# Performance work log

Measured on AMD Instinct MI355X. Metric: run time of the kernel, lower is better.

The kernel has to match this reference:

```python
import jax, jax.numpy as jnp
import numpy as np

B, LN, LT, D, DIN, H = 8, 64, 256, 1024, 2048, 4
LN_EPS = 1e-5
F16_EPS = float(np.finfo(np.float16).eps)


def setup_inputs() -> dict:
    key = jax.random.key(0)
    ks = jax.random.split(key, 16)
    n = lambda k, sh: jax.random.normal(k, sh, dtype=jnp.float32)
    s = 0.02
    z = lambda sh: jnp.zeros(sh, jnp.float32)
    return {
        "text_embeds": n(ks[0], (B, LT, D)),
        "node_embeds": n(ks[1], (B, LN, D)),
        "Wq": n(ks[2], (D, H * D)) * s, "bq": z((H * D,)),
        "Wk": n(ks[3], (D, H * D)) * s, "bk": z((H * D,)),
        "Wv": n(ks[4], (D, H * D)) * s, "bv": z((H * D,)),
        "Wo": n(ks[5], (H * D, D)) * s, "bo": z((D,)),
        "ln_g": jnp.ones((D,), jnp.float32), "ln_b": z((D,)),
        "aqW": n(ks[6], (D, D)) * s, "aqb": z((D,)),
        "akW": n(ks[7], (D, D)) * s, "akb": z((D,)),
        "att_v": n(ks[8], (D,)) * (1.0 / np.sqrt(D)),
        "att_b": z((D,)),
        "dp1W": n(ks[9], (D, DIN // 2)) * s, "dp1b": z((DIN // 2,)),
        "dp2W": n(ks[10], (DIN // 2, DIN)) * s, "dp2b": z((DIN,)),
        "gnn_mask": jax.random.randint(ks[11], (B, LN), 0, 2),
        "lm_mask": jax.random.randint(ks[12], (B, LT), 0, 2),
    }


def _forward(text_embeds, node_embeds, Wq, bq, Wk, bk, Wv, bv, Wo, bo, ln_g, ln_b,
             aqW, aqb, akW, akb, att_v, att_b, dp1W, dp1b, dp2W, dp2b,
             gnn_mask, lm_mask):
    x = node_embeds  # (B, LN, D)

    # ---- selfAttention_prompt: each of 4 heads has full width D ----
    def heads(w, b):
        return (x @ w + b).reshape(B, LN, H, D).transpose(0, 2, 1, 3)  # (B,H,LN,D)

    Q, K, V = heads(Wq, bq), heads(Wk, bk), heads(Wv, bv)
    A = jnp.einsum('bhqd,bhkd->bhqk', Q, K) / jnp.sqrt(jnp.float32(D))
    A = jnp.where(gnn_mask[:, None, None, :] == 0, -jnp.inf, A)
    alpha = jax.nn.softmax(A, axis=-1)
    out = jnp.einsum('bhqk,bhkd->bhqd', alpha, V)
    out = out.transpose(0, 2, 1, 3).reshape(B, LN, H * D)
    out = out @ Wo + bo + x
    # LayerNorm (torch default eps=1e-5)
    mu = out.mean(-1, keepdims=True)
    var = ((out - mu) ** 2).mean(-1, keepdims=True)
    H2 = (out - mu) / jnp.sqrt(var + LN_EPS) * ln_g + ln_b  # (B, LN, D)

    # ---- AdditiveAttention (Bahdanau): value_proj is unused in the original ----
    q = H2 @ aqW + aqb            # (B, LN, D)
    k = text_embeds @ akW + akb   # (B, LT, D)
    e = jnp.einsum('bqkd,d->bqk',
                   jnp.tanh(q[:, :, None, :] + k[:, None, :, :] + att_b), att_v)
    e = jnp.where(lm_mask[:, None, :] == 0, -jnp.inf, e)
    w = jax.nn.softmax(e, axis=-1)            # (B, LN, LT)
    H3 = jnp.einsum('bqk,bkd->bqd', w, text_embeds)  # context with raw V

    # ---- filter_Pool: masked mean over nodes ----
    m = gnn_mask.astype(H3.dtype)[:, :, None]
    cnt = jnp.clip(m.sum(1), F16_EPS, None)   # (B, 1)
    H4 = (H3 * m).sum(1) / cnt                # (B, D)

    # ---- domain projector (exact GELU like torch) ----
    Z = jax.nn.gelu(H4 @ dp1W + dp1b, approximate=False) @ dp2W + dp2b
    return Z  # (B, DIN)


def reference(text_embeds, node_embeds, Wq, bq, Wk, bk, Wv, bv, Wo, bo, ln_g, ln_b,
              aqW, aqb, akW, akb, att_v, att_b, dp1W, dp1b, dp2W, dp2b,
              gnn_mask, lm_mask):
    return _forward(text_embeds, node_embeds, Wq, bq, Wk, bk, Wv, bv, Wo, bo,
                    ln_g, ln_b, aqW, aqb, akW, akb, att_v, att_b,
                    dp1W, dp1b, dp2W, dp2b, gnn_mask, lm_mask)
```

## Files before the change

### kernel.cpp

```cpp
#include <hip/hip_runtime.h>
#include <hip/hip_bf16.h>
#include <math.h>

#define NB 8
#define LNN 64
#define LTN 256
#define DD 1024
#define NH 4
#define HDD 4096
#define DINN 2048
#define DHN 1024

#define C_TANH 2.8853900817779268f

typedef __bf16 bf16x8 __attribute__((ext_vector_type(8)));
typedef float f32x4 __attribute__((ext_vector_type(4)));

__device__ __forceinline__ ushort f2b(float f) {
  unsigned int u = __builtin_bit_cast(unsigned int, f);
  u = (u + 0x7FFFu + ((u >> 16) & 1u)) >> 16;
  return (ushort)u;
}

__global__ __launch_bounds__(256) void prep(const float* __restrict__ node,
                                            ushort* __restrict__ node_bf,
                                            const float* __restrict__ text,
                                            ushort* __restrict__ text_bf,
                                            const float* __restrict__ Wq,
                                            const float* __restrict__ Wk,
                                            const float* __restrict__ Wv,
                                            const float* __restrict__ Wo,
                                            const float* __restrict__ aqW,
                                            const float* __restrict__ akW,
                                            ushort* __restrict__ TwtQKV,
                                            ushort* __restrict__ TwtWo,
                                            ushort* __restrict__ TwtAQ) {
  int bid = blockIdx.x;
  int t = threadIdx.x;
  if (bid < 1280) {
    const float* in;
    ushort* out;
    int i;
    if (bid < 256) { in = node; out = node_bf; i = (bid * 256 + t) * 8; }
    else { in = text; out = text_bf; i = ((bid - 256) * 256 + t) * 8; }
    float4 a = *(const float4*)(in + i);
    float4 b = *(const float4*)(in + i + 4);
    ushort4 o0 = {f2b(a.x), f2b(a.y), f2b(a.z), f2b(a.w)};
    ushort4 o1 = {f2b(b.x), f2b(b.y), f2b(b.z), f2b(b.w)};
    *(ushort4*)(out + i) = o0;
    *(ushort4*)(out + i + 4) = o1;
    return;
  }
  bid -= 1280;
  const float* W;
  ushort* dst0;
  int K, N, tt;
  if (bid < 3072) {
    int z = bid >> 10;
    tt = bid & 1023;
    W = (z == 0) ? Wq : ((z == 1) ? Wk : Wv);
    dst0 = TwtQKV + (size_t)z * DD * HDD;
    K = DD; N = HDD;
  } else if (bid < 4096) {
    tt = bid - 3072; W = Wo; dst0 = TwtWo; K = HDD; N = DD;
  } else if (bid < 4352) {
    tt = bid - 4096; W = aqW; dst0 = TwtAQ; K = DD; N = DD;
  } else {
    tt = bid - 4352; W = akW; dst0 = TwtAQ + (size_t)DD * DD; K = DD; N = DD;
  }
  int ntn = N >> 6;
  int n0 = (tt % ntn) << 6, k0 = (tt / ntn) << 6;
  __shared__ float tf[64][65];
  int r = t >> 2, c4 = (t & 3) * 16;
  const float* src = W + (size_t)(k0 + r) * N + n0 + c4;
  float4 v0 = *(const float4*)(src);
  float4 v1 = *(const float4*)(src + 4);
  float4 v2 = *(const float4*)(src + 8);
  float4 v3 = *(const float4*)(src + 12);
  *(float4*)&tf[r][c4] = v0;
  *(float4*)&tf[r][c4 + 4] = v1;
  *(float4*)&tf[r][c4 + 8] = v2;
  *(float4*)&tf[r][c4 + 12] = v3;
  __syncthreads();
  int nl = t >> 2, kc = (t & 3) * 16;
  ushort tmp[16];
#pragma unroll
  for (int j = 0; j < 16; ++j) tmp[j] = f2b(tf[kc + j][nl]);
  ushort* dst = dst0 + (size_t)(n0 + nl) * K + k0 + kc;
  *(uint4*)(dst) = *(uint4*)&tmp[0];
  *(uint4*)(dst + 8) = *(uint4*)&tmp[8];
}

__global__ __launch_bounds__(256) void gemm_qkv3(const ushort* __restrict__ A,
                                                 const ushort* __restrict__ BtB,
                                                 const float* __restrict__ b0,
                                                 const float* __restrict__ b1,
                                                 const float* __restrict__ b2,
                                                 ushort* __restrict__ o0,
                                                 ushort* __restrict__ o1,
                                                 ushort* __restrict__ o2,
                                                 int M, int N, int K) {
  int z = blockIdx.z;
  const ushort* Bt = BtB + (size_t)z * N * K;
  const float* bias = (z == 0) ? b0 : ((z == 1) ? b1 : b2);
  ushort* Cout = (z == 0) ? o0 : ((z == 1) ? o1 : o2);
  __shared__ ushort Als[64 * 64];
  __shared__ ushort Bls[128 * 64];
  int tid = threadIdx.x;
  int m0 = blockIdx.y << 6, n0 = blockIdx.x << 7;
  int srow = tid >> 3, su = tid & 7;
  int sx = (su ^ (srow & 7)) * 8;
  const ushort* ga = A + (size_t)(m0 + srow) * K + su * 8;
  const ushort* gb = Bt + (size_t)(n0 + srow) * K + su * 8;
  int wa0 = srow * 64 + sx, wa1 = (srow + 32) * 64 + sx;
  int wb2 = (srow + 64) * 64 + sx, wb3 = (srow + 96) * 64 + sx;
  const size_t rs32 = (size_t)32 * K;
  int lane = tid & 63, w = tid >> 6;
  int wm = w >> 1, wn = w & 1;
  int r = lane & 15, kg = lane >> 4;
  f32x4 acc[2][4] = {};
  uint4 pa0 = *(const uint4*)(ga);
  uint4 pa1 = *(const uint4*)(ga + rs32);
  uint4 pb0 = *(const uint4*)(gb);
  uint4 pb1 = *(const uint4*)(gb + rs32);
  uint4 pb2 = *(const uint4*)(gb + 2 * rs32);
  uint4 pb3 = *(const uint4*)(gb + 3 * rs32);
  for (int k0 = 0; k0 < K; k0 += 64) {
    __syncthreads();
    *(uint4*)&Als[wa0] = pa0; *(uint4*)&Als[wa1] = pa1;
    *(uint4*)&Bls[wa0] = pb0; *(uint4*)&Bls[wa1] = pb1;
    *(uint4*)&Bls[wb2] = pb2; *(uint4*)&Bls[wb3] = pb3;
    __syncthreads();
    int kn = k0 + 64;
    if (kn < K) {
      pa0 = *(const uint4*)(ga + kn);
      pa1 = *(const uint4*)(ga + rs32 + kn);
      pb0 = *(const uint4*)(gb + kn);
      pb1 = *(const uint4*)(gb + rs32 + kn);
      pb2 = *(const uint4*)(gb + 2 * rs32 + kn);
      pb3 = *(const uint4*)(gb + 3 * rs32 + kn);
    }
#pragma unroll
    for (int h = 0; h < 2; ++h) {
      int sa = ((h * 4 + kg) ^ (r & 7)) * 8;
      bf16x8 af[2], bfr[4];
#pragma unroll
      for (int m = 0; m < 2; ++m)
        af[m] = *(const bf16x8*)&Als[(wm * 32 + m * 16 + r) * 64 + sa];
#pragma unroll
      for (int n = 0; n < 4; ++n)
        bfr[n] = *(const bf16x8*)&Bls[(wn * 64 + n * 16 + r) * 64 + sa];
#pragma unroll
      for (int m = 0; m < 2; ++m)
#pragma unroll
        for (int n = 0; n < 4; ++n)
          acc[m][n] = __builtin_amdgcn_mfma_f32_16x16x32_bf16(af[m], bfr[n], acc[m][n], 0, 0, 0);
    }
  }
#pragma unroll
  for (int m = 0; m < 2; ++m)
#pragma unroll
    for (int n = 0; n < 4; ++n) {
      f32x4 a = acc[m][n];
#pragma unroll
      for (int v = 0; v < 4; ++v) {
        int row = m0 + wm * 32 + m * 16 + kg * 4 + v;
        int col = n0 + wn * 64 + n * 16 + r;
        Cout[(size_t)row * N + col] = f2b(a[v] + bias[col]);
      }
    }
}

__global__ __launch_bounds__(256) void gemm_wo_split(const ushort* __restrict__ A,
                                                     const ushort* __restrict__ Bt,
                                                     float* __restrict__ P,
                                                     int M, int N, int K) {
  __shared__ ushort Als[64 * 64];
  __shared__ ushort Bls[128 * 64];
  int tid = threadIdx.x;
  int m0 = blockIdx.y << 6, n0 = blockIdx.x << 7;
  int Ks = K >> 2, kbase = blockIdx.z * Ks;
  int srow = tid >> 3, su = tid & 7;
  int sx = (su ^ (srow & 7)) * 8;
  const ushort* ga = A + (size_t)(m0 + srow) * K + kbase + su * 8;
  const ushort* gb = Bt + (size_t)(n0 + srow) * K + kbase + su * 8;
  int wa0 = srow * 64 + sx, wa1 = (srow + 32) * 64 + sx;
  int wb2 = (srow + 64) * 64 + sx, wb3 = (srow + 96) * 64 + sx;
  const size_t rs32 = (size_t)32 * K;
  int lane = tid & 63, w = tid >> 6;
  int wm = w >> 1, wn = w & 1;
  int r = lane & 15, kg = lane >> 4;
  f32x4 acc[2][4] = {};
  uint4 pa0 = *(const uint4*)(ga);
  uint4 pa1 = *(const uint4*)(ga + rs32);
  uint4 pb0 = *(const uint4*)(gb);
  uint4 pb1 = *(const uint4*)(gb + rs32);
  uint4 pb2 = *(const uint4*)(gb + 2 * rs32);
  uint4 pb3 = *(const uint4*)(gb + 3 * rs32);
  for (int k0 = 0; k0 < Ks; k0 += 64) {
    __syncthreads();
    *(uint4*)&Als[wa0] = pa0; *(uint4*)&Als[wa1] = pa1;
    *(uint4*)&Bls[wa0] = pb0; *(uint4*)&Bls[wa1] = pb1;
    *(uint4*)&Bls[wb2] = pb2; *(uint4*)&Bls[wb3] = pb3;
    __syncthreads();
    int kn = k0 + 64;
    if (kn < Ks) {
      pa0 = *(const uint4*)(ga + kn);
      pa1 = *(const uint4*)(ga + rs32 + kn);
      pb0 = *(const uint4*)(gb + kn);
      pb1 = *(const uint4*)(gb + rs32 + kn);
      pb2 = *(const uint4*)(gb + 2 * rs32 + kn);
      pb3 = *(const uint4*)(gb + 3 * rs32 + kn);
    }
#pragma unroll
    for (int h = 0; h < 2; ++h) {
      int sa = ((h * 4 + kg) ^ (r & 7)) * 8;
      bf16x8 af[2], bfr[4];
#pragma unroll
      for (int m = 0; m < 2; ++m)
        af[m] = *(const bf16x8*)&Als[(wm * 32 + m * 16 + r) * 64 + sa];
#pragma unroll
      for (int n = 0; n < 4; ++n)
        bfr[n] = *(const bf16x8*)&Bls[(wn * 64 + n * 16 + r) * 64 + sa];
#pragma unroll
      for (int m = 0; m < 2; ++m)
#pragma unroll
        for (int n = 0; n < 4; ++n)
          acc[m][n] = __builtin_amdgcn_mfma_f32_16x16x32_bf16(af[m], bfr[n], acc[m][n], 0, 0, 0);
    }
  }
#pragma unroll
  for (int m = 0; m < 2; ++m)
#pragma unroll
    for (int n = 0; n < 4; ++n) {
      f32x4 a = acc[m][n];
#pragma unroll
      for (int v = 0; v < 4; ++v) {
        int row = m0 + wm * 32 + m * 16 + kg * 4 + v;
        int col = n0 + wn * 64 + n * 16 + r;
        P[((size_t)blockIdx.z * M + row) * N + col] = a[v];
      }
    }
}

__global__ __launch_bounds__(256) void gemm_aqak(const ushort* __restrict__ H2,
                                                 const ushort* __restrict__ Tbf,
                                                 const ushort* __restrict__ TwtAQ,
                                                 const float* __restrict__ aqb,
                                                 const float* __restrict__ akb,
                                                 const float* __restrict__ attb,
                                                 float* __restrict__ QBu,
                                                 float* __restrict__ KAB,
                                                 int N, int K) {
  __shared__ ushort Als[64 * 64];
  __shared__ ushort Bls[128 * 64];
  int tid = threadIdx.x;
  int gm0 = blockIdx.y << 6, n0 = blockIdx.x << 7;
  const ushort* Abase;
  const ushort* Bt;
  const float* bias;
  const float* bias2;
  float* Obase;
  if (gm0 < 512) {
    Abase = H2 + (size_t)gm0 * K;
    Bt = TwtAQ;
    bias = aqb; bias2 = nullptr;
    Obase = QBu + (size_t)gm0 * N;
  } else {
    Abase = Tbf + (size_t)(gm0 - 512) * K;
    Bt = TwtAQ + (size_t)N * K;
    bias = akb; bias2 = attb;
    Obase = KAB + (size_t)(gm0 - 512) * N;
  }
  int srow = tid >> 3, su = tid & 7;
  int sx = (su ^ (srow & 7)) * 8;
  const ushort* ga = Abase + (size_t)srow * K + su * 8;
  const ushort* gb = Bt + (size_t)(n0 + srow) * K + su * 8;
  int wa0 = srow * 64 + sx, wa1 = (srow + 32) * 64 + sx;
  int wb2 = (srow + 64) * 64 + sx, wb3 = (srow + 96) * 64 + sx;
  const size_t rs32 = (size_t)32 * K;
  int lane = tid & 63, w = tid >> 6;
  int wm = w >> 1, wn = w & 1;
  int r = lane & 15, kg = lane >> 4;
  f32x4 acc[2][4] = {};
  uint4 pa0 = *(const uint4*)(ga);
  uint4 pa1 = *(const uint4*)(ga + rs32);
  uint4 pb0 = *(const uint4*)(gb);
  uint4 pb1 = *(const uint4*)(gb + rs32);
  uint4 pb2 = *(const uint4*)(gb + 2 * rs32);
  uint4 pb3 = *(const uint4*)(gb + 3 * rs32);
  for (int k0 = 0; k0 < K; k0 += 64) {
    __syncthreads();
    *(uint4*)&Als[wa0] = pa0; *(uint4*)&Als[wa1] = pa1;
    *(uint4*)&Bls[wa0] = pb0; *(uint4*)&Bls[wa1] = pb1;
    *(uint4*)&Bls[wb2] = pb2; *(uint4*)&Bls[wb3] = pb3;
    __syncthreads();
    int kn = k0 + 64;
    if (kn < K) {
      pa0 = *(const uint4*)(ga + kn);
      pa1 = *(const uint4*)(ga + rs32 + kn);
      pb0 = *(const uint4*)(gb + kn);
      pb1 = *(const uint4*)(gb + rs32 + kn);
      pb2 = *(const uint4*)(gb + 2 * rs32 + kn);
      pb3 = *(const uint4*)(gb + 3 * rs32 + kn);
    }
#pragma unroll
    for (int h = 0; h < 2; ++h) {
      int sa = ((h * 4 + kg) ^ (r & 7)) * 8;
      bf16x8 af[2], bfr[4];
#pragma unroll
      for (int m = 0; m < 2; ++m)
        af[m] = *(const bf16x8*)&Als[(wm * 32 + m * 16 + r) * 64 + sa];
#pragma unroll
      for (int n = 0; n < 4; ++n)
        bfr[n] = *(const bf16x8*)&Bls[(wn * 64 + n * 16 + r) * 64 + sa];
#pragma unroll
      for (int m = 0; m < 2; ++m)
#pragma unroll
        for (int n = 0; n < 4; ++n)
          acc[m][n] = __builtin_amdgcn_mfma_f32_16x16x32_bf16(af[m], bfr[n], acc[m][n], 0, 0, 0);
    }
  }
#pragma unroll
  for (int m = 0; m < 2; ++m)
#pragma unroll
    for (int n = 0; n < 4; ++n) {
      f32x4 a = acc[m][n];
#pragma unroll
      for (int v = 0; v < 4; ++v) {
        int lrow = wm * 32 + m * 16 + kg * 4 + v;
        int col = n0 + wn * 64 + n * 16 + r;
        float x = a[v] + bias[col];
        if (bias2) x += bias2[col];
        Obase[(size_t)lrow * N + col] = x * C_TANH;
      }
    }
}

__global__ __launch_bounds__(256) void wo_ln(const float* __restrict__ P,
                                             const float* __restrict__ bo,
                                             const float* __restrict__ node,
                                             const float* __restrict__ g,
                                             const float* __restrict__ be,
                                             ushort* __restrict__ Y) {
  int row = blockIdx.x, tid = threadIdx.x;
  int c = tid * 4;
  const size_t MN = (size_t)512 * 1024;
  size_t o = (size_t)row * DD + c;
  float4 v0 = *(const float4*)(P + o);
  float4 v1 = *(const float4*)(P + MN + o);
  float4 v2 = *(const float4*)(P + 2 * MN + o);
  float4 v3 = *(const float4*)(P + 3 * MN + o);
  float4 rv = *(const float4*)(node + o);
  float4 bv = *(const float4*)(bo + c);
  float4 v;
  v.x = v0.x + v1.x + v2.x + v3.x + rv.x + bv.x;
  v.y = v0.y + v1.y + v2.y + v3.y + rv.y + bv.y;
  v.z = v0.z + v1.z + v2.z + v3.z + rv.z + bv.z;
  v.w = v0.w + v1.w + v2.w + v3.w + rv.w + bv.w;
  float s = v.x + v.y + v.z + v.w;
  float ss = v.x * v.x + v.y * v.y + v.z * v.z + v.w * v.w;
  for (int o2 = 32; o2; o2 >>= 1) {
    s += __shfl_xor(s, o2, 64);
    ss += __shfl_xor(ss, o2, 64);
  }
  __shared__ float rb_[8];
  int lane = tid & 63, w = tid >> 6;
  if (lane == 0) { rb_[w] = s; rb_[4 + w] = ss; }
  __syncthreads();
  s = rb_[0] + rb_[1] + rb_[2] + rb_[3];
  ss = rb_[4] + rb_[5] + rb_[6] + rb_[7];
  float mu = s * (1.f / 1024.f);
  float var = ss * (1.f / 1024.f) - mu * mu;
  float rstd = rsqrtf(var + 1e-5f);
  ushort4 o4;
  o4.x = f2b((v.x - mu) * rstd * g[c + 0] + be[c + 0]);
  o4.y = f2b((v.y - mu) * rstd * g[c + 1] + be[c + 1]);
  o4.z = f2b((v.z - mu) * rstd * g[c + 2] + be[c + 2]);
  o4.w = f2b((v.w - mu) * rstd * g[c + 3] + be[c + 3]);
  *(ushort4*)(Y + (size_t)row * DD + c) = o4;
}

__global__ __launch_bounds__(256) void attn_qk(const ushort* __restrict__ Qb,
                                               const ushort* __restrict__ Kb,
                                               float* __restrict__ Sp) {
  int bh = blockIdx.x, ks = blockIdx.y;
  int b = bh >> 2;
  size_t base = ((size_t)b * LNN) * HDD + (size_t)(bh & 3) * DD + ks * 128;
  __shared__ ushort Als[64 * 64];
  __shared__ ushort Bls[64 * 64];
  int tid = threadIdx.x;
  int srow = tid >> 2, su0 = (tid & 3) * 2;
  const ushort* ga = Qb + base + (size_t)srow * HDD + su0 * 8;
  const ushort* gb = Kb + base + (size_t)srow * HDD + su0 * 8;
  int wa0 = srow * 64 + ((su0) ^ (srow & 7)) * 8;
  int wa1 = srow * 64 + ((su0 + 1) ^ (srow & 7)) * 8;
  int lane = tid & 63, w = tid >> 6;
  int wm = w >> 1, wn = w & 1;
  int r = lane & 15, kg = lane >> 4;
  f32x4 acc[2][2] = {};
  uint4 pa0 = *(const uint4*)(ga);
  uint4 pa1 = *(const uint4*)(ga + 8);
  uint4 pb0 = *(const uint4*)(gb);
  uint4 pb1 = *(const uint4*)(gb + 8);
  for (int k0 = 0; k0 < 128; k0 += 64) {
    __syncthreads();
    *(uint4*)&Als[wa0] = pa0; *(uint4*)&Als[wa1] = pa1;
    *(uint4*)&Bls[wa0] = pb0; *(uint4*)&Bls[wa1] = pb1;
    __syncthreads();
    if (k0 == 0) {
      pa0 = *(const uint4*)(ga + 64);
      pa1 = *(const uint4*)(ga + 64 + 8);
      pb0 = *(const uint4*)(gb + 64);
      pb1 = *(const uint4*)(gb + 64 + 8);
    }
#pragma unroll
    for (int h = 0; h < 2; ++h) {
      int sa = ((h * 4 + kg) ^ (r & 7)) * 8;
      bf16x8 af[2], bfr[2];
#pragma unroll
      for (int m = 0; m < 2; ++m)
        af[m] = *(const bf16x8*)&Als[(wm * 32 + m * 16 + r) * 64 + sa];
#pragma unroll
      for (int n = 0; n < 2; ++n)
        bfr[n] = *(const bf16x8*)&Bls[(wn * 32 + n * 16 + r) * 64 + sa];
#pragma unroll
      for (int m = 0; m < 2; ++m)
#pragma unroll
        for (int n = 0; n < 2; ++n)
          acc[m][n] = __builtin_amdgcn_mfma_f32_16x16x32_bf16(af[m], bfr[n], acc[m][n], 0, 0, 0);
    }
  }
  float* out = Sp + ((size_t)ks * 32 + bh) * 4096;
#pragma unroll
  for (int m = 0; m < 2; ++m)
#pragma unroll
    for (int n = 0; n < 2; ++n) {
      f32x4 a = acc[m][n];
#pragma unroll
      for (int v = 0; v < 4; ++v) {
        int row = wm * 32 + m * 16 + kg * 4 + v;
        int col = wn * 32 + n * 16 + r;
        out[row * 64 + col] = a[v];
      }
    }
}

__global__ __launch_bounds__(256) void attn_pv(const float* __restrict__ Sp,
                                               const ushort* __restrict__ Vb,
                                               const int* __restrict__ gmask,
                                               ushort* __restrict__ AO) {
  int bid = blockIdx.x;
  int bh = bid >> 3, dt = bid & 7;
  int b = bh >> 2;
  int d0 = dt * 128;
  size_t base = ((size_t)b * LNN) * HDD + (size_t)(bh & 3) * DD;
  __shared__ float S[64][68];
  __shared__ ushort Pls[64 * 72];
  __shared__ ushort Vt[128 * 72];
  int tid = threadIdx.x;
  int lane = tid & 63, w = tid >> 6;
  {
    int fbase = tid * 16;
    float a[16];
#pragma unroll
    for (int i = 0; i < 16; i += 4) {
      float4 v = *(const float4*)(Sp + (size_t)bh * 4096 + fbase + i);
      a[i] = v.x; a[i + 1] = v.y; a[i + 2] = v.z; a[i + 3] = v.w;
    }
#pragma unroll
    for (int ks = 1; ks < 8; ++ks) {
      const float* p = Sp + ((size_t)ks * 32 + bh) * 4096 + fbase;
#pragma unroll
      for (int i = 0; i < 16; i += 4) {
        float4 v = *(const float4*)(p + i);
        a[i] += v.x; a[i + 1] += v.y; a[i + 2] += v.z; a[i + 3] += v.w;
      }
    }
    int q = fbase >> 6, k = fbase & 63;
#pragma unroll
    for (int i = 0; i < 16; ++i) S[q][k + i] = a[i];
  }
  {
    int kq = lane, dq = w * 32;
    const ushort* src = Vb + base + (size_t)kq * HDD + d0 + dq;
    uint4 v0 = *(const uint4*)src;
    uint4 v1 = *(const uint4*)(src + 8);
    uint4 v2 = *(const uint4*)(src + 16);
    uint4 v3 = *(const uint4*)(src + 24);
    ushort tmp[32];
    *(uint4*)&tmp[0] = v0; *(uint4*)&tmp[8] = v1;
    *(uint4*)&tmp[16] = v2; *(uint4*)&tmp[24] = v3;
#pragma unroll
    for (int j = 0; j < 32; ++j) Vt[(dq + j) * 72 + kq] = tmp[j];
  }
  __syncthreads();
  bool valid = gmask[b * LNN + lane] != 0;
  for (int i = 0; i < 16; ++i) {
    int q = w * 16 + i;
    float v = valid ? S[q][lane] * 0.03125f : -__builtin_inff();
    float mx = v;
    for (int o = 32; o; o >>= 1) mx = fmaxf(mx, __shfl_xor(mx, o, 64));
    float e = valid ? __expf(v - mx) : 0.f;
    float s = e;
    for (int o = 32; o; o >>= 1) s += __shfl_xor(s, o, 64);
    Pls[q * 72 + lane] = f2b(__fdividef(e, s));
  }
  __syncthreads();
  int wm = w >> 1, wn = w & 1;
  int r = lane & 15, kg = lane >> 4;
  f32x4 acc[2][4] = {};
#pragma unroll
  for (int h = 0; h < 2; ++h) {
    int ko = h * 32 + kg * 8;
    bf16x8 af[2], bfr[4];
#pragma unroll
    for (int m = 0; m < 2; ++m)
      af[m] = *(const bf16x8*)&Pls[(wm * 32 + m * 16 + r) * 72 + ko];
#pragma unroll
    for (int n = 0; n < 4; ++n)
      bfr[n] = *(const bf16x8*)&Vt[(wn * 64 + n * 16 + r) * 72 + ko];
#pragma unroll
    for (int m = 0; m < 2; ++m)
#pragma unroll
      for (int n = 0; n < 4; ++n)
        acc[m][n] = __builtin_amdgcn_mfma_f32_16x16x32_bf16(af[m], bfr[n], acc[m][n], 0, 0, 0);
  }
#pragma unroll
  for (int m = 0; m < 2; ++m)
#pragma unroll
    for (int n = 0; n < 4; ++n) {
      f32x4 a = acc[m][n];
#pragma unroll
      for (int v = 0; v < 4; ++v) {
        int q = wm * 32 + m * 16 + kg * 4 + v;
        int col = wn * 64 + n * 16 + r;
        AO[base + (size_t)q * HDD + d0 + col] = f2b(a[v]);
      }
    }
}

__global__ __launch_bounds__(256) void addatt_e(const float* __restrict__ QBu,
                                                const float* __restrict__ KAB,
                                                const float* __restrict__ av_,
                                                float* __restrict__ E8) {
  int ds = blockIdx.x, qt = blockIdx.y, b = blockIdx.z;
  int tid = threadIdx.x;
  __shared__ float qs[8][128];
  __shared__ float avs[128];
  __shared__ float red[4];
  int bq0 = b * LNN + qt * 8;
  {
    int qq = tid >> 5, dd = (tid & 31) * 4;
    *(float4*)&qs[qq][dd] = *(const float4*)(QBu + (size_t)(bq0 + qq) * DD + ds * 128 + dd);
  }
  float av = (tid < 128) ? av_[ds * 128 + tid] : 0.f;
  if (tid < 128) avs[tid] = av;
  float s = av;
  for (int o = 32; o; o >>= 1) s += __shfl_xor(s, o, 64);
  int lane = tid & 63, w = tid >> 6;
  if (lane == 0) red[w] = s;
  __syncthreads();
  float sumav = red[0] + red[1] + red[2] + red[3];
  const float* kr = KAB + (size_t)(b * LTN + tid) * DD + ds * 128;
  float ac[8] = {};
#pragma unroll 2
  for (int d = 0; d < 128; d += 4) {
    float4 kv = *(const float4*)(kr + d);
    float4 av4 = *(const float4*)&avs[d];
#pragma unroll
    for (int qq = 0; qq < 8; ++qq) {
      float4 q4 = *(const float4*)&qs[qq][d];
      ac[qq] = fmaf(av4.x, __builtin_amdgcn_rcpf(__builtin_amdgcn_exp2f(q4.x + kv.x) + 1.f), ac[qq]);
      ac[qq] = fmaf(av4.y, __builtin_amdgcn_rcpf(__builtin_amdgcn_exp2f(q4.y + kv.y) + 1.f), ac[qq]);
      ac[qq] = fmaf(av4.z, __builtin_amdgcn_rcpf(__builtin_amdgcn_exp2f(q4.z + kv.z) + 1.f), ac[qq]);
      ac[qq] = fmaf(av4.w, __builtin_amdgcn_rcpf(__builtin_amdgcn_exp2f(q4.w + kv.w) + 1.f), ac[qq]);
    }
  }
  size_t ebase = ((size_t)ds * 512 + bq0) * LTN + tid;
#pragma unroll
  for (int qq = 0; qq < 8; ++qq)
    E8[ebase + (size_t)qq * LTN] = sumav - 2.f * ac[qq];
}

__global__ __launch_bounds__(256) void addatt_sm(const float* __restrict__ E8,
                                                 const int* __restrict__ lmask,
                                                 float* __restrict__ Wv) {
  int bq = blockIdx.x;
  int b = bq >> 6;
  int tid = threadIdx.x;
  __shared__ float rb_[8];
  float e = 0.f;
#pragma unroll
  for (int ks = 0; ks < 8; ++ks)
    e += E8[((size_t)ks * 512 + bq) * LTN + tid];
  bool valid = lmask[b * LTN + tid] != 0;
  float v = valid ? e : -__builtin_inff();
  int lane = tid & 63, w = tid >> 6;
  float m = v;
  for (int o = 32; o; o >>= 1) m = fmaxf(m, __shfl_xor(m, o, 64));
  if (lane == 0) rb_[w] = m;
  __syncthreads();
  m = fmaxf(fmaxf(rb_[0], rb_[1]), fmaxf(rb_[2], rb_[3]));
  float ex = valid ? __expf(v - m) : 0.f;
  float sm = ex;
  for (int o = 32; o; o >>= 1) sm += __shfl_xor(sm, o, 64);
  if (lane == 0) rb_[4 + w] = sm;
  __syncthreads();
  sm = rb_[4] + rb_[5] + rb_[6] + rb_[7];
  Wv[(size_t)bq * LTN + tid] = __fdividef(ex, sm);
}

__global__ __launch_bounds__(256) void addatt_pool(const float* __restrict__ Wv,
                                                   const float* __restrict__ text,
                                                   const int* __restrict__ gmask,
                                                   float* __restrict__ H4) {
  int dt = blockIdx.x, b = blockIdx.y;
  int tid = threadIdx.x;
  __shared__ float cf[LTN];
  float c = 0.f, cnt = 0.f;
#pragma unroll 8
  for (int q = 0; q < LNN; ++q) {
    float m = (gmask[b * LNN + q] != 0) ? 1.f : 0.f;
    cnt += m;
    c = fmaf(m, Wv[(size_t)(b * LNN + q) * LTN + tid], c);
  }
  cf[tid] = c;
  cnt = fmaxf(cnt, 9.765625e-04f);
  __syncthreads();
  int d = dt * 256 + tid;
  const float* tb = text + (size_t)b * LTN * DD + d;
  float acc = 0.f;
#pragma unroll 8
  for (int k = 0; k < LTN; ++k) acc = fmaf(cf[k], tb[(size_t)k * DD], acc);
  H4[b * DD + d] = acc / cnt;
}

__global__ __launch_bounds__(256) void dp_split(const float* __restrict__ X,
                                                const float* __restrict__ W,
                                                float* __restrict__ P,
                                                int K, int N) {
  int jt = blockIdx.x, kt = blockIdx.y;
  int t = threadIdx.x;
  __shared__ float xs[8][32];
  if (t < 64) {
    int b = t >> 3, kk = (t & 7) * 4;
    *(float4*)&xs[b][kk] = *(const float4*)(X + (size_t)b * K + kt * 32 + kk);
  }
  __syncthreads();
  int j = jt * 64 + (t & 63);
  int bg = (t >> 6) * 2;
  const float* wp = W + (size_t)(kt * 32) * N + j;
  float a0 = 0.f, a1 = 0.f;
#pragma unroll
  for (int k = 0; k < 32; ++k) {
    float w = wp[(size_t)k * N];
    a0 = fmaf(xs[bg + 0][k], w, a0);
    a1 = fmaf(xs[bg + 1][k], w, a1);
  }
  P[((size_t)kt * 8 + bg + 0) * N + j] = a0;
  P[((size_t)kt * 8 + bg + 1) * N + j] = a1;
}

__global__ __launch_bounds__(256) void dp_split2g(const float* __restrict__ P1,
                                                  const float* __restrict__ b1,
                                                  const float* __restrict__ W,
                                                  float* __restrict__ P,
                                                  int K, int N) {
  int jt = blockIdx.x, kt = blockIdx.y;
  int t = threadIdx.x;
  __shared__ float xs[8][32];
  {
    int b = t >> 5, kk = t & 31;
    int j = kt * 32 + kk;
    float s = b1[j];
#pragma unroll 8
    for (int p = 0; p < 32; ++p) s += P1[((size_t)p * 8 + b) * K + j];
    xs[b][kk] = 0.5f * s * (1.f + erff(s * 0.70710678118654752440f));
  }
  __syncthreads();
  int j = jt * 64 + (t & 63);
  int bg = (t >> 6) * 2;
  const float* wp = W + (size_t)(kt * 32) * N + j;
  float a0 = 0.f, a1 = 0.f;
#pragma unroll
  for (int k = 0; k < 32; ++k) {
    float w = wp[(size_t)k * N];
    a0 = fmaf(xs[bg + 0][k], w, a0);
    a1 = fmaf(xs[bg + 1][k], w, a1);
  }
  P[((size_t)kt * 8 + bg + 0) * N + j] = a0;
  P[((size_t)kt * 8 + bg + 1) * N + j] = a1;
}

template <int GELU>
__global__ __launch_bounds__(256) void dp_reduce(const float* __restrict__ P,
                                                 const float* __restrict__ bias,
                                                 float* __restrict__ O, int N) {
  int b = blockIdx.y;
  int j = blockIdx.x * 256 + threadIdx.x;
  float s = bias[j];
#pragma unroll 8
  for (int kt = 0; kt < 32; ++kt) s += P[((size_t)kt * 8 + b) * N + j];
  if constexpr (GELU) s = 0.5f * s * (1.f + erff(s * 0.70710678118654752440f));
  O[(size_t)b * N + j] = s;
}

extern "C" void kernel_launch(void* const* d_in, const int* in_sizes, int n_in,
                              void* d_out, int out_size, void* d_ws, size_t ws_size,
                              hipStream_t stream) {
  const float* text = (const float*)d_in[0];
  const float* node = (const float*)d_in[1];
  const float* Wq = (const float*)d_in[2];
  const float* bq = (const float*)d_in[3];
  const float* Wk = (const float*)d_in[4];
  const float* bk = (const float*)d_in[5];
  const float* Wv = (const float*)d_in[6];
  const float* bv = (const float*)d_in[7];
  const float* Wo = (const float*)d_in[8];
  const float* bo = (const float*)d_in[9];
  const float* lng = (const float*)d_in[10];
  const float* lnb = (const float*)d_in[11];
  const float* aqW = (const float*)d_in[12];
  const float* aqb = (const float*)d_in[13];
  const float* akW = (const float*)d_in[14];
  const float* akb = (const float*)d_in[15];
  const float* attv = (const float*)d_in[16];
  const float* attb = (const float*)d_in[17];
  const float* dp1W = (const float*)d_in[18];
  const float* dp1b = (const float*)d_in[19];
  const float* dp2W = (const float*)d_in[20];
  const float* dp2b = (const float*)d_in[21];
  const int* gmask = (const int*)d_in[22];
  const int* lmask = (const int*)d_in[23];
  (void)in_sizes; (void)n_in; (void)out_size; (void)ws_size;

  char* base = (char*)d_ws;
#define MB(x) (((size_t)(x)) << 20)
  ushort* TwtQKV = (ushort*)(base);
  ushort* TwtWo = (ushort*)(base + MB(24));
  ushort* TwtAQ = (ushort*)(base + MB(32));
  ushort* node_bf = (ushort*)(base + MB(36));
  ushort* text_bf = (ushort*)(base + MB(37));
  ushort* Qb = (ushort*)(base + MB(41));
  ushort* Kb = (ushort*)(base + MB(45));
  ushort* Vb = (ushort*)(base + MB(49));
  ushort* AO = (ushort*)(base + MB(53));
  float* Sp = (float*)(base + MB(57));
  float* P_Wo = (float*)(base + MB(61));
  ushort* H2 = (ushort*)(base + MB(69));
  float* QBu = (float*)(base + MB(70));
  float* KAB = (float*)(base + MB(72));
  float* E8 = (float*)(base + MB(80));
  float* Wvb = (float*)(base + MB(84));
  float* H4 = (float*)(base + MB(84) + (512 << 10));
  float* P1 = (float*)(base + MB(85));
  float* P2 = (float*)(base + MB(86));
  float* Z = (float*)d_out;
#undef MB

  const int M1 = NB * LNN;
  dim3 blk(256);

  prep<<<dim3(5888), blk, 0, stream>>>(node, node_bf, text, text_bf,
                                       Wq, Wk, Wv, Wo, aqW, akW,
                                       TwtQKV, TwtWo, TwtAQ);

  gemm_qkv3<<<dim3(HDD / 128, M1 / 64, 3), blk, 0, stream>>>(node_bf, TwtQKV, bq, bk, bv, Qb, Kb, Vb, M1, HDD, DD);

  attn_qk<<<dim3(NB * NH, 8), blk, 0, stream>>>(Qb, Kb, Sp);
  attn_pv<<<dim3(NB * NH * 8), blk, 0, stream>>>(Sp, Vb, gmask, AO);

  gemm_wo_split<<<dim3(DD / 128, M1 / 64, 4), blk, 0, stream>>>(AO, TwtWo, P_Wo, M1, DD, HDD);
  wo_ln<<<dim3(M1), blk, 0, stream>>>(P_Wo, bo, node, lng, lnb, H2);

  gemm_aqak<<<dim3(DD / 128, 40), blk, 0, stream>>>(H2, text_bf, TwtAQ, aqb, akb, attb, QBu, KAB, DD, DD);

  addatt_e<<<dim3(8, 8, NB), blk, 0, stream>>>(QBu, KAB, attv, E8);
  addatt_sm<<<dim3(M1), blk, 0, stream>>>(E8, lmask, Wvb);
  addatt_pool<<<dim3(4, NB), blk, 0, stream>>>(Wvb, text, gmask, H4);

  dp_split<<<dim3(DHN / 64, 32), blk, 0, stream>>>(H4, dp1W, P1, DD, DHN);
  dp_split2g<<<dim3(DINN / 64, 32), blk, 0, stream>>>(P1, dp1b, dp2W, P2, DHN, DINN);
  dp_reduce<0><<<dim3(DINN / 256, NB), blk, 0, stream>>>(P2, dp2b, Z, DINN);
}
```

Before: 162.0 us.

## Fuse self-attention QK and PV kernels and fuse additive softmax with pooling

Merges attn_qk and attn_pv into one kernel. Each block now computes the full 64x64 QK^T over the whole 1024-wide head before the softmax and PV product, which removes the split-K partial buffer and one launch. In exchange, the QK^T work is repeated 8 times across the d-tiles. It also merges the additive-attention softmax and the masked mean-pool into one kernel with one block per batch. That block loops serially over the 64 query rows and then over 4 d-tiles. This drops the intermediate weight buffer and a launch, but leaves only 8 blocks to do all of that work.

Result: slower. 258.8 us (+59.8%).

```diff
diff --git a/kernel.cpp b/kernel.cpp
--- a/kernel.cpp
+++ b/kernel.cpp
@@ -381,105 +381,72 @@
   *(ushort4*)(Y + (size_t)row * DD + c) = o4;
 }
 
-__global__ __launch_bounds__(256) void attn_qk(const ushort* __restrict__ Qb,
-                                               const ushort* __restrict__ Kb,
-                                               float* __restrict__ Sp) {
-  int bh = blockIdx.x, ks = blockIdx.y;
-  int b = bh >> 2;
-  size_t base = ((size_t)b * LNN) * HDD + (size_t)(bh & 3) * DD + ks * 128;
-  __shared__ ushort Als[64 * 64];
-  __shared__ ushort Bls[64 * 64];
-  int tid = threadIdx.x;
-  int srow = tid >> 2, su0 = (tid & 3) * 2;
-  const ushort* ga = Qb + base + (size_t)srow * HDD + su0 * 8;
-  const ushort* gb = Kb + base + (size_t)srow * HDD + su0 * 8;
-  int wa0 = srow * 64 + ((su0) ^ (srow & 7)) * 8;
-  int wa1 = srow * 64 + ((su0 + 1) ^ (srow & 7)) * 8;
-  int lane = tid & 63, w = tid >> 6;
-  int wm = w >> 1, wn = w & 1;
-  int r = lane & 15, kg = lane >> 4;
-  f32x4 acc[2][2] = {};
-  uint4 pa0 = *(const uint4*)(ga);
-  uint4 pa1 = *(const uint4*)(ga + 8);
-  uint4 pb0 = *(const uint4*)(gb);
-  uint4 pb1 = *(const uint4*)(gb + 8);
-  for (int k0 = 0; k0 < 128; k0 += 64) {
-    __syncthreads();
-    *(uint4*)&Als[wa0] = pa0; *(uint4*)&Als[wa1] = pa1;
-    *(uint4*)&Bls[wa0] = pb0; *(uint4*)&Bls[wa1] = pb1;
-    __syncthreads();
-    if (k0 == 0) {
-      pa0 = *(const uint4*)(ga + 64);
-      pa1 = *(const uint4*)(ga + 64 + 8);
-      pb0 = *(const uint4*)(gb + 64);
-      pb1 = *(const uint4*)(gb + 64 + 8);
-    }
-#pragma unroll
-    for (int h = 0; h < 2; ++h) {
-      int sa = ((h * 4 + kg) ^ (r & 7)) * 8;
-      bf16x8 af[2], bfr[2];
-#pragma unroll
-      for (int m = 0; m < 2; ++m)
-        af[m] = *(const bf16x8*)&Als[(wm * 32 + m * 16 + r) * 64 + sa];
-#pragma unroll
-      for (int n = 0; n < 2; ++n)
-        bfr[n] = *(const bf16x8*)&Bls[(wn * 32 + n * 16 + r) * 64 + sa];
-#pragma unroll
-      for (int m = 0; m < 2; ++m)
-#pragma unroll
-        for (int n = 0; n < 2; ++n)
-          acc[m][n] = __builtin_amdgcn_mfma_f32_16x16x32_bf16(af[m], bfr[n], acc[m][n], 0, 0, 0);
-    }
-  }
-  float* out = Sp + ((size_t)ks * 32 + bh) * 4096;
-#pragma unroll
-  for (int m = 0; m < 2; ++m)
-#pragma unroll
-    for (int n = 0; n < 2; ++n) {
-      f32x4 a = acc[m][n];
-#pragma unroll
-      for (int v = 0; v < 4; ++v) {
-        int row = wm * 32 + m * 16 + kg * 4 + v;
-        int col = wn * 32 + n * 16 + r;
-        out[row * 64 + col] = a[v];
-      }
-    }
-}
-
-__global__ __launch_bounds__(256) void attn_pv(const float* __restrict__ Sp,
-                                               const ushort* __restrict__ Vb,
-                                               const int* __restrict__ gmask,
-                                               ushort* __restrict__ AO) {
+__global__ __launch_bounds__(256) void attn_one(const ushort* __restrict__ Qb,
+                                                const ushort* __restrict__ Kb,
+                                                const ushort* __restrict__ Vb,
+                                                const int* __restrict__ gmask,
+                                                ushort* __restrict__ AO) {
   int bid = blockIdx.x;
   int bh = bid >> 3, dt = bid & 7;
   int b = bh >> 2;
   int d0 = dt * 128;
   size_t base = ((size_t)b * LNN) * HDD + (size_t)(bh & 3) * DD;
+  __shared__ ushort Als[64 * 64];
+  __shared__ ushort Bls[64 * 64];
   __shared__ float S[64][68];
   __shared__ ushort Pls[64 * 72];
   __shared__ ushort Vt[128 * 72];
   int tid = threadIdx.x;
   int lane = tid & 63, w = tid >> 6;
+  int wm = w >> 1, wn = w & 1;
+  int r = lane & 15, kg = lane >> 4;
   {
-    int fbase = tid * 16;
-    float a[16];
-#pragma unroll
-    for (int i = 0; i < 16; i += 4) {
-      float4 v = *(const float4*)(Sp + (size_t)bh * 4096 + fbase + i);
-      a[i] = v.x; a[i + 1] = v.y; a[i + 2] = v.z; a[i + 3] = v.w;
-    }
-#pragma unroll
-    for (int ks = 1; ks < 8; ++ks) {
-      const float* p = Sp + ((size_t)ks * 32 + bh) * 4096 + fbase;
-#pragma unroll
-      for (int i = 0; i < 16; i += 4) {
-        float4 v = *(const float4*)(p + i);
-        a[i] += v.x; a[i + 1] += v.y; a[i + 2] += v.z; a[i + 3] += v.w;
+    int srow = tid >> 2, su0 = (tid & 3) * 2;
+    const ushort* ga = Qb + base + (size_t)srow * HDD + su0 * 8;
+    const ushort* gb = Kb + base + (size_t)srow * HDD + su0 * 8;
+    int wa0 = srow * 64 + ((su0) ^ (srow & 7)) * 8;
+    int wa1 = srow * 64 + ((su0 + 1) ^ (srow & 7)) * 8;
+    f32x4 acc[2][2] = {};
+    uint4 pa0 = *(const uint4*)(ga);
+    uint4 pa1 = *(const uint4*)(ga + 8);
+    uint4 pb0 = *(const uint4*)(gb);
+    uint4 pb1 = *(const uint4*)(gb + 8);
+    for (int k0 = 0; k0 < DD; k0 += 64) {
+      __syncthreads();
+      *(uint4*)&Als[wa0] = pa0; *(uint4*)&Als[wa1] = pa1;
+      *(uint4*)&Bls[wa0] = pb0; *(uint4*)&Bls[wa1] = pb1;
+      __syncthreads();
+      int kn = k0 + 64;
+      if (kn < DD) {
+        pa0 = *(const uint4*)(ga + kn);
+        pa1 = *(const uint4*)(ga + kn + 8);
+        pb0 = *(const uint4*)(gb + kn);
+        pb1 = *(const uint4*)(gb + kn + 8);
       }
-    }
-    int q = fbase >> 6, k = fbase & 63;
-#pragma unroll
-    for (int i = 0; i < 16; ++i) S[q][k + i] = a[i];
+#pragma unroll
+      for (int h = 0; h < 2; ++h) {
+        int sa = ((h * 4 + kg) ^ (r & 7)) * 8;
+        bf16x8 af[2], bfr[2];
+#pragma unroll
+        for (int m = 0; m < 2; ++m)
+          af[m] = *(const bf16x8*)&Als[(wm * 32 + m * 16 + r) * 64 + sa];
+#pragma unroll
+        for (int n = 0; n < 2; ++n)
+          bfr[n] = *(const bf16x8*)&Bls[(wn * 32 + n * 16 + r) * 64 + sa];
+#pragma unroll
+        for (int m = 0; m < 2; ++m)
+#pragma unroll
+          for (int n = 0; n < 2; ++n)
+            acc[m][n] = __builtin_amdgcn_mfma_f32_16x16x32_bf16(af[m], bfr[n], acc[m][n], 0, 0, 0);
+      }
+    }
+#pragma unroll
+    for (int m = 0; m < 2; ++m)
+#pragma unroll
+      for (int n = 0; n < 2; ++n)
+#pragma unroll
+        for (int v = 0; v < 4; ++v)
+          S[wm * 32 + m * 16 + kg * 4 + v][wn * 32 + n * 16 + r] = acc[m][n][v];
   }
   {
     int kq = lane, dq = w * 32;
@@ -507,8 +474,6 @@
     Pls[q * 72 + lane] = f2b(__fdividef(e, s));
   }
   __syncthreads();
-  int wm = w >> 1, wn = w & 1;
-  int r = lane & 15, kg = lane >> 4;
   f32x4 acc[2][4] = {};
 #pragma unroll
   for (int h = 0; h < 2; ++h) {
@@ -583,57 +548,53 @@
     E8[ebase + (size_t)qq * LTN] = sumav - 2.f * ac[qq];
 }
 
-__global__ __launch_bounds__(256) void addatt_sm(const float* __restrict__ E8,
-                                                 const int* __restrict__ lmask,
-                                                 float* __restrict__ Wv) {
-  int bq = blockIdx.x;
-  int b = bq >> 6;
-  int tid = threadIdx.x;
-  __shared__ float rb_[8];
-  float e = 0.f;
-#pragma unroll
-  for (int ks = 0; ks < 8; ++ks)
-    e += E8[((size_t)ks * 512 + bq) * LTN + tid];
-  bool valid = lmask[b * LTN + tid] != 0;
-  float v = valid ? e : -__builtin_inff();
-  int lane = tid & 63, w = tid >> 6;
-  float m = v;
-  for (int o = 32; o; o >>= 1) m = fmaxf(m, __shfl_xor(m, o, 64));
-  if (lane == 0) rb_[w] = m;
-  __syncthreads();
-  m = fmaxf(fmaxf(rb_[0], rb_[1]), fmaxf(rb_[2], rb_[3]));
-  float ex = valid ? __expf(v - m) : 0.f;
-  float sm = ex;
-  for (int o = 32; o; o >>= 1) sm += __shfl_xor(sm, o, 64);
-  if (lane == 0) rb_[4 + w] = sm;
-  __syncthreads();
-  sm = rb_[4] + rb_[5] + rb_[6] + rb_[7];
-  Wv[(size_t)bq * LTN + tid] = __fdividef(ex, sm);
-}
-
-__global__ __launch_bounds__(256) void addatt_pool(const float* __restrict__ Wv,
-                                                   const float* __restrict__ text,
-                                                   const int* __restrict__ gmask,
-                                                   float* __restrict__ H4) {
-  int dt = blockIdx.x, b = blockIdx.y;
+__global__ __launch_bounds__(256) void addatt_smpool(const float* __restrict__ E8,
+                                                     const int* __restrict__ lmask,
+                                                     const float* __restrict__ text,
+                                                     const int* __restrict__ gmask,
+                                                     float* __restrict__ H4) {
+  int b = blockIdx.x;
   int tid = threadIdx.x;
   __shared__ float cf[LTN];
-  float c = 0.f, cnt = 0.f;
+  __shared__ float rb_[8];
+  int lane = tid & 63, w = tid >> 6;
+  bool valid = lmask[b * LTN + tid] != 0;
+  float cnt = 0.f;
+#pragma unroll
+  for (int q = 0; q < LNN; ++q) cnt += (gmask[b * LNN + q] != 0) ? 1.f : 0.f;
+  cnt = fmaxf(cnt, 9.765625e-04f);
+  float coeff = 0.f;
+  for (int q = 0; q < LNN; ++q) {
+    int bq = b * LNN + q;
+    float e = 0.f;
+#pragma unroll
+    for (int ks = 0; ks < 8; ++ks)
+      e += E8[((size_t)ks * 512 + bq) * LTN + tid];
+    float v = valid ? e : -__builtin_inff();
+    float m = v;
+    for (int o = 32; o; o >>= 1) m = fmaxf(m, __shfl_xor(m, o, 64));
+    if (lane == 0) rb_[w] = m;
+    __syncthreads();
+    m = fmaxf(fmaxf(rb_[0], rb_[1]), fmaxf(rb_[2], rb_[3]));
+    float ex = valid ? __expf(v - m) : 0.f;
+    float sm = ex;
+    for (int o = 32; o; o >>= 1) sm += __shfl_xor(sm, o, 64);
+    if (lane == 0) rb_[4 + w] = sm;
+    __syncthreads();
+    sm = rb_[4] + rb_[5] + rb_[6] + rb_[7];
+    if (gmask[bq] != 0) coeff += __fdividef(ex, sm);
+  }
+  cf[tid] = coeff;
+  __syncthreads();
+  const float* tb = text + (size_t)b * LTN * DD;
+#pragma unroll
+  for (int dt = 0; dt < 4; ++dt) {
+    int d = dt * 256 + tid;
+    float acc = 0.f;
 #pragma unroll 8
-  for (int q = 0; q < LNN; ++q) {
-    float m = (gmask[b * LNN + q] != 0) ? 1.f : 0.f;
-    cnt += m;
-    c = fmaf(m, Wv[(size_t)(b * LNN + q) * LTN + tid], c);
-  }
-  cf[tid] = c;
-  cnt = fmaxf(cnt, 9.765625e-04f);
-  __syncthreads();
-  int d = dt * 256 + tid;
-  const float* tb = text + (size_t)b * LTN * DD + d;
-  float acc = 0.f;
-#pragma unroll 8
-  for (int k = 0; k < LTN; ++k) acc = fmaf(cf[k], tb[(size_t)k * DD], acc);
-  H4[b * DD + d] = acc / cnt;
+    for (int k = 0; k < LTN; ++k) acc = fmaf(cf[k], tb[(size_t)k * DD + d], acc);
+    H4[b * DD + d] = acc / cnt;
+  }
 }
 
 __global__ __launch_bounds__(256) void dp_split(const float* __restrict__ X,
@@ -746,13 +707,11 @@
   ushort* Kb = (ushort*)(base + MB(45));
   ushort* Vb = (ushort*)(base + MB(49));
   ushort* AO = (ushort*)(base + MB(53));
-  float* Sp = (float*)(base + MB(57));
   float* P_Wo = (float*)(base + MB(61));
   ushort* H2 = (ushort*)(base + MB(69));
   float* QBu = (float*)(base + MB(70));
   float* KAB = (float*)(base + MB(72));
   float* E8 = (float*)(base + MB(80));
-  float* Wvb = (float*)(base + MB(84));
   float* H4 = (float*)(base + MB(84) + (512 << 10));
   float* P1 = (float*)(base + MB(85));
   float* P2 = (float*)(base + MB(86));
@@ -768,8 +727,7 @@
 
   gemm_qkv3<<<dim3(HDD / 128, M1 / 64, 3), blk, 0, stream>>>(node_bf, TwtQKV, bq, bk, bv, Qb, Kb, Vb, M1, HDD, DD);
 
-  attn_qk<<<dim3(NB * NH, 8), blk, 0, stream>>>(Qb, Kb, Sp);
-  attn_pv<<<dim3(NB * NH * 8), blk, 0, stream>>>(Sp, Vb, gmask, AO);
+  attn_one<<<dim3(NB * NH * 8), blk, 0, stream>>>(Qb, Kb, Vb, gmask, AO);
 
   gemm_wo_split<<<dim3(DD / 128, M1 / 64, 4), blk, 0, stream>>>(AO, TwtWo, P_Wo, M1, DD, HDD);
   wo_ln<<<dim3(M1), blk, 0, stream>>>(P_Wo, bo, node, lng, lnb, H2);
@@ -777,8 +735,7 @@
   gemm_aqak<<<dim3(DD / 128, 40), blk, 0, stream>>>(H2, text_bf, TwtAQ, aqb, akb, attb, QBu, KAB, DD, DD);
 
   addatt_e<<<dim3(8, 8, NB), blk, 0, stream>>>(QBu, KAB, attv, E8);
-  addatt_sm<<<dim3(M1), blk, 0, stream>>>(E8, lmask, Wvb);
-  addatt_pool<<<dim3(4, NB), blk, 0, stream>>>(Wvb, text, gmask, H4);
+  addatt_smpool<<<dim3(NB), blk, 0, stream>>>(E8, lmask, text, gmask, H4);
 
   dp_split<<<dim3(DHN / 64, 32), blk, 0, stream>>>(H4, dp1W, P1, DD, DHN);
   dp_split2g<<<dim3(DINN / 64, 32), blk, 0, stream>>>(P1, dp1b, dp2W, P2, DHN, DINN);
```
